# Kernel tuning notes

Hardware: AMD Instinct MI355X
Metric: run time of the kernel (lower is better)

Reference implementation:

```python
import jax, jax.numpy as jnp
import numpy as np

NQ = 4          # n_qubits
NL = 2          # ansatz layers in timestep circuit
T = 200         # n_timesteps
DEG = 3         # qsvt_degree
B = 2048        # batch
NROTS = 5 * NQ * NL     # 40
QFF_NROTS = 5 * NQ      # 20
DIM = 2 ** NQ

# --- batched 2x2 gate matrices (h = theta/2, shape (N,)) ---
def _rx(h):
    c = jnp.cos(h).astype(jnp.complex64)
    s = (-1j * jnp.sin(h)).astype(jnp.complex64)
    return jnp.stack([jnp.stack([c, s], -1), jnp.stack([s, c], -1)], -2)

def _ry(h):
    c, s = jnp.cos(h), jnp.sin(h)
    return jnp.stack([jnp.stack([c, -s], -1), jnp.stack([s, c], -1)], -2).astype(jnp.complex64)

def _rz(h):
    e = jnp.exp(-1j * h.astype(jnp.complex64))
    z = jnp.zeros_like(e)
    return jnp.stack([jnp.stack([e, z], -1), jnp.stack([z, jnp.conj(e)], -1)], -2)

# state layout: (N, 2, 2, ..., 2) with axis 1+w = qubit w (PennyLane wire ordering)
def _apply_1q(state, mat, w):
    st = jnp.moveaxis(state, 1 + w, -1)
    st = jnp.einsum('bij,b...j->b...i', mat, st)
    return jnp.moveaxis(st, -1, 1 + w)

def _apply_crx(state, h, cw, tw):
    m = _rx(h)
    st = jnp.moveaxis(state, (1 + cw, 1 + tw), (-2, -1))  # (..., control, target)
    s1 = jnp.einsum('bij,b...j->b...i', m, st[..., 1, :])  # RX on target iff control=1
    st = jnp.stack([st[..., 0, :], s1], axis=-2)
    return jnp.moveaxis(st, (-2, -1), (1 + cw, 1 + tw))

def _ansatz(state, params, layers):
    # params: (N, 5*NQ*layers) float
    half = params * 0.5
    idx = 0
    for _ in range(layers):
        for i in range(NQ):
            state = _apply_1q(state, _rx(half[:, idx]), i)
            state = _apply_1q(state, _ry(half[:, idx + 1]), i)
            state = _apply_1q(state, _rz(half[:, idx + 2]), i)
            idx += 3
        for i in range(NQ):
            state = _apply_crx(state, half[:, idx], i, (i + 1) % NQ)
            idx += 1
        for i in range(NQ - 1, -1, -1):
            state = _apply_crx(state, half[:, idx], i, (i - 1) % NQ)
            idx += 1
    return state

def _lcu(base, tparams, coeffs):
    # base: (B, DIM) complex; tparams: (B, T, NROTS); coeffs: (B, T) complex
    b, t, r = tparams.shape
    flat = tparams.reshape(b * t, r)
    st = jnp.repeat(base, t, axis=0).reshape((b * t,) + (2,) * NQ)
    st = _ansatz(st, flat, NL)
    ev = st.reshape(b, t, DIM)
    return jnp.einsum('bti,bt->bi', ev, coeffs)

def _expvals(state):
    # returns (B, 3*NQ): [<X_0..X_{n-1}>, <Y...>, <Z...>]
    outs_x, outs_y, outs_z = [], [], []
    red = tuple(range(1, NQ))  # reduce all non-batch, non-target axes after moveaxis
    for i in range(NQ):
        st = jnp.moveaxis(state, 1 + i, -1)
        s0, s1 = st[..., 0], st[..., 1]
        z = jnp.conj(s0) * s1
        outs_x.append(jnp.sum(2.0 * jnp.real(z), axis=red))
        outs_y.append(jnp.sum(2.0 * jnp.imag(z), axis=red))
        outs_z.append(jnp.sum(jnp.abs(s0) ** 2 - jnp.abs(s1) ** 2, axis=red))
    return jnp.stack(outs_x + outs_y + outs_z, axis=1).astype(jnp.float32)

def _forward(timestep_params, poly_coeffs, mix_re, mix_im, qff_params):
    b = timestep_params.shape[0]
    base = jnp.zeros((b, DIM), jnp.complex64).at[:, 0].set(1.0)
    coeffs = jnp.broadcast_to((mix_re + 1j * mix_im).astype(jnp.complex64), (b, T))
    # QSVT polynomial: acc = sum_k c_k (LCU)^k |0>
    acc = poly_coeffs[0] * base
    work = base
    for k in range(1, DEG + 1):
        work = _lcu(work, timestep_params, coeffs)
        acc = acc + poly_coeffs[k] * work
    acc = acc / jnp.sum(jnp.abs(poly_coeffs))  # L1 norm of poly coeffs
    norm = jnp.linalg.norm(acc, axis=1, keepdims=True)
    st = (acc / (norm + 1e-9)).reshape((b,) + (2,) * NQ)
    qp = jnp.broadcast_to(qff_params, (b, QFF_NROTS))
    st = _ansatz(st, qp, 1)
    return _expvals(st)

def setup_inputs() -> dict:
    key = jax.random.key(0)
    k1, k2, k3, k4, k5 = jax.random.split(key, 5)
    return {
        'timestep_params': jax.random.uniform(k1, (B, T, NROTS), jnp.float32),
        'poly_coeffs': jax.random.uniform(k2, (DEG + 1,), jnp.float32),
        'mix_re': jax.random.uniform(k3, (T,), jnp.float32),
        'mix_im': jax.random.uniform(k4, (T,), jnp.float32),
        'qff_params': jax.random.uniform(k5, (QFF_NROTS,), jnp.float32),
    }

def reference(timestep_params, poly_coeffs, mix_re, mix_im, qff_params):
    return _forward(timestep_params, poly_coeffs, mix_re, mix_im, qff_params)
```

## Files before the change

kernel.cpp:

```cpp
#include <hip/hip_runtime.h>
#include <math.h>

#define TSTEPS 200
#define NROTS  40
#define BLK    256
#define DEG    3

typedef float f2 __attribute__((ext_vector_type(2)));

__device__ __forceinline__ void fsc(float h, float& s, float& c) {
    s = __sinf(h); c = __cosf(h);
}

__device__ __forceinline__ f2 crot(f2 a) { return (f2){-a.y, a.x}; }

__device__ __forceinline__ void make_u(float h1, float h2, float h3, float* u) {
    float s1, c1, s2, c2, s3, c3;
    fsc(h1, s1, c1); fsc(h2, s2, c2); fsc(h3, s3, c3);
    float A = c1 * c2, Bv = s1 * s2, C = c1 * s2, D = s1 * c2;
    u[0] =  c3 * A + s3 * Bv;
    u[1] =  c3 * Bv - s3 * A;
    u[2] = -(c3 * C + s3 * D);
    u[3] =  s3 * C - c3 * D;
}

template<int BIT>
__device__ __forceinline__ void g_u2(f2* A, const float* u) {
    const float u00r = u[0], u00i = u[1], u01r = u[2], u01i = u[3];
    #pragma unroll
    for (int p = 0; p < 16; ++p) {
        if (p & BIT) continue;
        const int q = p | BIT;
        f2 a0 = A[p], a1 = A[q];
        f2 r0 = crot(a0), r1 = crot(a1);
        A[p] =  u00r * a0 + u00i * r0 + u01r * a1 + u01i * r1;
        A[q] =  u00r * a1 - u00i * r1 - u01r * a0 + u01i * r0;
    }
}

template<int CBIT, int TBIT>
__device__ __forceinline__ void g_crx_pre(f2* A, float s, float c) {
    #pragma unroll
    for (int p = 0; p < 16; ++p) {
        if (!(p & CBIT) || (p & TBIT)) continue;
        const int q = p | TBIT;
        f2 a0 = A[p], a1 = A[q];
        A[p] = c * a0 - s * crot(a1);
        A[q] = c * a1 - s * crot(a0);
    }
}

__device__ __forceinline__ void apply_layer_pre(f2* A, const float (&u)[4][4],
                                                const float (&cs)[8][2]) {
    g_u2<8>(A, u[0]); g_u2<4>(A, u[1]); g_u2<2>(A, u[2]); g_u2<1>(A, u[3]);
    g_crx_pre<8, 4>(A, cs[0][0], cs[0][1]);
    g_crx_pre<4, 2>(A, cs[1][0], cs[1][1]);
    g_crx_pre<2, 1>(A, cs[2][0], cs[2][1]);
    g_crx_pre<1, 8>(A, cs[3][0], cs[3][1]);
    g_crx_pre<1, 2>(A, cs[4][0], cs[4][1]);
    g_crx_pre<2, 4>(A, cs[5][0], cs[5][1]);
    g_crx_pre<4, 8>(A, cs[6][0], cs[6][1]);
    g_crx_pre<8, 1>(A, cs[7][0], cs[7][1]);
}

template<int S, int HALF>
__device__ __forceinline__ void rstep(f2* A, int lane) {
    const bool hi = (lane >> S) & 1;
    #pragma unroll
    for (int j = 0; j < HALF; ++j) {
        f2 send = hi ? A[j] : A[j + HALF];
        f2 keep = hi ? A[j + HALF] : A[j];
        f2 got;
        got.x = __shfl_xor(send.x, 1 << S, 64);
        got.y = __shfl_xor(send.y, 1 << S, 64);
        A[j] = keep + got;
    }
}

extern "C" __global__ void __launch_bounds__(BLK)
qac_kernel(const float* __restrict__ tp,
           const float* __restrict__ poly,
           const float* __restrict__ mixr,
           const float* __restrict__ mixi,
           const float* __restrict__ qff,
           float* __restrict__ out)
{
    __shared__ f2 s_red[4][16];
    __shared__ f2 s_w[16];
    __shared__ f2 s_acc[16];

    const int b    = blockIdx.x;
    const int tid  = threadIdx.x;
    const int lane = tid & 63;
    const int wv   = tid >> 6;

    if (tid < 16) {
        s_w[tid]   = (f2){tid == 0 ? 1.f : 0.f, 0.f};
        s_acc[tid] = (f2){tid == 0 ? poly[0] : 0.f, 0.f};
    }

    float cr_ = 0.f, ci_ = 0.f;
    if (tid < TSTEPS) { cr_ = mixr[tid]; ci_ = mixi[tid]; }
    const int mt = (tid < TSTEPS) ? tid : (TSTEPS - 1);
    const float4* p4 = (const float4*)(tp + (size_t)b * (TSTEPS * NROTS) + mt * NROTS);

    float tu[2][4][4];
    float tc[2][8][2];
    #pragma unroll
    for (int L = 0; L < 2; ++L) {
        float4 f0 = p4[5*L+0], f1 = p4[5*L+1], f2v = p4[5*L+2], f3 = p4[5*L+3], f4 = p4[5*L+4];
        make_u(0.5f*f0.x,  0.5f*f0.y,  0.5f*f0.z,  tu[L][0]);
        make_u(0.5f*f0.w,  0.5f*f1.x,  0.5f*f1.y,  tu[L][1]);
        make_u(0.5f*f1.z,  0.5f*f1.w,  0.5f*f2v.x, tu[L][2]);
        make_u(0.5f*f2v.y, 0.5f*f2v.z, 0.5f*f2v.w, tu[L][3]);
        fsc(0.5f*f3.x, tc[L][0][0], tc[L][0][1]);
        fsc(0.5f*f3.y, tc[L][1][0], tc[L][1][1]);
        fsc(0.5f*f3.z, tc[L][2][0], tc[L][2][1]);
        fsc(0.5f*f3.w, tc[L][3][0], tc[L][3][1]);
        fsc(0.5f*f4.x, tc[L][4][0], tc[L][4][1]);
        fsc(0.5f*f4.y, tc[L][5][0], tc[L][5][1]);
        fsc(0.5f*f4.z, tc[L][6][0], tc[L][6][1]);
        fsc(0.5f*f4.w, tc[L][7][0], tc[L][7][1]);
    }

    const int vidx = ((lane & 1) << 3) | ((lane & 2) << 1) | ((lane & 4) >> 1) | ((lane & 8) >> 3);

    __syncthreads();

    #pragma unroll 1
    for (int k = 1; k <= DEG; ++k) {
        f2 A[16];
        #pragma unroll
        for (int i = 0; i < 16; ++i) A[i] = s_w[i];

        apply_layer_pre(A, tu[0], tc[0]);
        apply_layer_pre(A, tu[1], tc[1]);

        #pragma unroll
        for (int i = 0; i < 16; ++i) A[i] = cr_ * A[i] + ci_ * crot(A[i]);

        rstep<0, 8>(A, lane);
        rstep<1, 4>(A, lane);
        rstep<2, 2>(A, lane);
        rstep<3, 1>(A, lane);
        f2 tot = A[0];
        tot.x += __shfl_xor(tot.x, 16, 64); tot.y += __shfl_xor(tot.y, 16, 64);
        tot.x += __shfl_xor(tot.x, 32, 64); tot.y += __shfl_xor(tot.y, 32, 64);
        if (lane < 16) s_red[wv][vidx] = tot;

        __syncthreads();
        if (tid < 16) {
            f2 r = s_red[0][tid] + s_red[1][tid] + s_red[2][tid] + s_red[3][tid];
            s_w[tid] = r;
            s_acc[tid] += poly[k] * r;
        }
        __syncthreads();
    }

    if (tid < 16) {
        const int l = tid;
        float l1 = fabsf(poly[0]) + fabsf(poly[1]) + fabsf(poly[2]) + fabsf(poly[3]);
        float inv = 1.f / l1;
        float ar = s_acc[l].x * inv, ai = s_acc[l].y * inv;
        float n2 = ar * ar + ai * ai;
        #pragma unroll
        for (int o = 1; o < 16; o <<= 1) n2 += __shfl_xor(n2, o, 64);
        float sc = 1.f / (sqrtf(n2) + 1e-9f);
        ar *= sc; ai *= sc;

        float s, c, pr, pi, se, ce, t0;
        #pragma unroll
        for (int w = 0; w < 4; ++w) {
            const int BIT = 8 >> w;
            fsc(0.5f * qff[3 * w + 0], s, c);
            pr = __shfl_xor(ar, BIT, 64); pi = __shfl_xor(ai, BIT, 64);
            t0 = c * ar + s * pi; ai = c * ai - s * pr; ar = t0;
            fsc(0.5f * qff[3 * w + 1], s, c);
            pr = __shfl_xor(ar, BIT, 64); pi = __shfl_xor(ai, BIT, 64);
            se = (l & BIT) ? s : -s;
            t0 = c * ar + se * pr; ai = c * ai + se * pi; ar = t0;
            fsc(0.5f * qff[3 * w + 2], s, c);
            se = (l & BIT) ? s : -s;
            t0 = c * ar - se * ai; ai = c * ai + se * ar; ar = t0;
        }
        #define CRXF(CB, TB, hp) { fsc(0.5f * (hp), s, c);                        \
            pr = __shfl_xor(ar, TB, 64); pi = __shfl_xor(ai, TB, 64);             \
            ce = (l & CB) ? c : 1.f; se = (l & CB) ? s : 0.f;                     \
            t0 = ce * ar + se * pi; ai = ce * ai - se * pr; ar = t0; }
        CRXF(8, 4, qff[12]) CRXF(4, 2, qff[13]) CRXF(2, 1, qff[14]) CRXF(1, 8, qff[15])
        CRXF(1, 2, qff[16]) CRXF(2, 4, qff[17]) CRXF(4, 8, qff[18]) CRXF(8, 1, qff[19])
        #undef CRXF

        float* o = out + (size_t)b * 12;
        #pragma unroll
        for (int w = 0; w < 4; ++w) {
            const int BIT = 8 >> w;
            pr = __shfl_xor(ar, BIT, 64); pi = __shfl_xor(ai, BIT, 64);
            float m = (l & BIT) ? 0.f : 1.f;
            float X = m * 2.f * (ar * pr + ai * pi);
            float Y = m * 2.f * (ar * pi - ai * pr);
            float Z = m * (ar * ar + ai * ai - pr * pr - pi * pi);
            #pragma unroll
            for (int of = 1; of < 16; of <<= 1) {
                X += __shfl_xor(X, of, 64);
                Y += __shfl_xor(Y, of, 64);
                Z += __shfl_xor(Z, of, 64);
            }
            if (l == 0) { o[w] = X; o[4 + w] = Y; o[8 + w] = Z; }
        }
    }
}

extern "C" void kernel_launch(void* const* d_in, const int* in_sizes, int n_in,
                              void* d_out, int out_size, void* d_ws, size_t ws_size,
                              hipStream_t stream) {
    const float* tp   = (const float*)d_in[0];
    const float* poly = (const float*)d_in[1];
    const float* mixr = (const float*)d_in[2];
    const float* mixi = (const float*)d_in[3];
    const float* qff  = (const float*)d_in[4];
    float* out = (float*)d_out;
    const int B = in_sizes[0] / (TSTEPS * NROTS);
    qac_kernel<<<dim3(B), dim3(BLK), 0, stream>>>(tp, poly, mixr, mixi, qff, out);
}
```

Baseline: 163.1 us.

## Switch state to split real/imag planes packed in pairs for packed FP32 math

Each thread's 16-amplitude state moves from interleaved complex values to separate real and imaginary planes. Each two-float vector now holds two neighbouring amplitudes, so gates on the upper three qubits can run as two-wide packed FP32 multiply-adds. Gates that act within a pair (qubit bit 1) get dedicated scalar routines, and the shared-memory accumulator is read back in planar order. The aim is to cut VALU instruction count in the gate-simulation loop, which dominates the kernel. The cost is more complex indexing and some extra lane extract/insert work for the intra-pair gates.

```diff
diff --git a/kernel.cpp b/kernel.cpp
--- a/kernel.cpp
+++ b/kernel.cpp
@@ -6,13 +6,13 @@
 #define BLK    256
 #define DEG    3
 
-typedef float f2 __attribute__((ext_vector_type(2)));
+typedef float f2v __attribute__((ext_vector_type(2)));
+
+__device__ __forceinline__ f2v vs(float x) { return (f2v){x, x}; }
 
 __device__ __forceinline__ void fsc(float h, float& s, float& c) {
     s = __sinf(h); c = __cosf(h);
 }
-
-__device__ __forceinline__ f2 crot(f2 a) { return (f2){-a.y, a.x}; }
 
 __device__ __forceinline__ void make_u(float h1, float h2, float h3, float* u) {
     float s1, c1, s2, c2, s3, c3;
@@ -24,56 +24,103 @@
     u[3] =  s3 * C - c3 * D;
 }
 
-template<int BIT>
-__device__ __forceinline__ void g_u2(f2* A, const float* u) {
+template<int PB>
+__device__ __forceinline__ void g_u2_pk(f2v* R, f2v* I, const float* u) {
+    const f2v u00r = vs(u[0]), u00i = vs(u[1]), u01r = vs(u[2]), u01i = vs(u[3]);
+    #pragma unroll
+    for (int pj = 0; pj < 8; ++pj) {
+        if (pj & PB) continue;
+        const int qj = pj | PB;
+        f2v a0r = R[pj], a0i = I[pj], a1r = R[qj], a1i = I[qj];
+        R[pj] =  u00r*a0r - u00i*a0i + u01r*a1r - u01i*a1i;
+        I[pj] =  u00r*a0i + u00i*a0r + u01r*a1i + u01i*a1r;
+        R[qj] = -(u01r*a0r) - u01i*a0i + u00r*a1r + u00i*a1i;
+        I[qj] = -(u01r*a0i) + u01i*a0r + u00r*a1i - u00i*a1r;
+    }
+}
+
+__device__ __forceinline__ void g_u2_b1(f2v* R, f2v* I, const float* u) {
     const float u00r = u[0], u00i = u[1], u01r = u[2], u01i = u[3];
     #pragma unroll
-    for (int p = 0; p < 16; ++p) {
-        if (p & BIT) continue;
-        const int q = p | BIT;
-        f2 a0 = A[p], a1 = A[q];
-        f2 r0 = crot(a0), r1 = crot(a1);
-        A[p] =  u00r * a0 + u00i * r0 + u01r * a1 + u01i * r1;
-        A[q] =  u00r * a1 - u00i * r1 - u01r * a0 + u01i * r0;
-    }
-}
-
-template<int CBIT, int TBIT>
-__device__ __forceinline__ void g_crx_pre(f2* A, float s, float c) {
-    #pragma unroll
-    for (int p = 0; p < 16; ++p) {
-        if (!(p & CBIT) || (p & TBIT)) continue;
-        const int q = p | TBIT;
-        f2 a0 = A[p], a1 = A[q];
-        A[p] = c * a0 - s * crot(a1);
-        A[q] = c * a1 - s * crot(a0);
-    }
-}
-
-__device__ __forceinline__ void apply_layer_pre(f2* A, const float (&u)[4][4],
-                                                const float (&cs)[8][2]) {
-    g_u2<8>(A, u[0]); g_u2<4>(A, u[1]); g_u2<2>(A, u[2]); g_u2<1>(A, u[3]);
-    g_crx_pre<8, 4>(A, cs[0][0], cs[0][1]);
-    g_crx_pre<4, 2>(A, cs[1][0], cs[1][1]);
-    g_crx_pre<2, 1>(A, cs[2][0], cs[2][1]);
-    g_crx_pre<1, 8>(A, cs[3][0], cs[3][1]);
-    g_crx_pre<1, 2>(A, cs[4][0], cs[4][1]);
-    g_crx_pre<2, 4>(A, cs[5][0], cs[5][1]);
-    g_crx_pre<4, 8>(A, cs[6][0], cs[6][1]);
-    g_crx_pre<8, 1>(A, cs[7][0], cs[7][1]);
+    for (int j = 0; j < 8; ++j) {
+        float a0r = R[j].x, a0i = I[j].x, a1r = R[j].y, a1i = I[j].y;
+        R[j].x =  u00r*a0r - u00i*a0i + u01r*a1r - u01i*a1i;
+        I[j].x =  u00r*a0i + u00i*a0r + u01r*a1i + u01i*a1r;
+        R[j].y = -u01r*a0r - u01i*a0i + u00r*a1r + u00i*a1i;
+        I[j].y = -u01r*a0i + u01i*a0r + u00r*a1i - u00i*a1r;
+    }
+}
+
+template<int PC, int PT>
+__device__ __forceinline__ void g_crx_pk(f2v* R, f2v* I, float s, float c) {
+    const f2v sv = vs(s), cv = vs(c);
+    #pragma unroll
+    for (int pj = 0; pj < 8; ++pj) {
+        if (!(pj & PC) || (pj & PT)) continue;
+        const int qj = pj | PT;
+        f2v a0r = R[pj], a0i = I[pj], a1r = R[qj], a1i = I[qj];
+        R[pj] = cv*a0r + sv*a1i;
+        I[pj] = cv*a0i - sv*a1r;
+        R[qj] = cv*a1r + sv*a0i;
+        I[qj] = cv*a1i - sv*a0r;
+    }
+}
+
+template<int JC>
+__device__ __forceinline__ void g_crx_t1(f2v* R, f2v* I, float s, float c) {
+    #pragma unroll
+    for (int j = 0; j < 8; ++j) {
+        if (!(j & JC)) continue;
+        float a0r = R[j].x, a0i = I[j].x, a1r = R[j].y, a1i = I[j].y;
+        R[j].x = c*a0r + s*a1i;
+        I[j].x = c*a0i - s*a1r;
+        R[j].y = c*a1r + s*a0i;
+        I[j].y = c*a1i - s*a0r;
+    }
+}
+
+template<int PT>
+__device__ __forceinline__ void g_crx_c1(f2v* R, f2v* I, float s, float c) {
+    #pragma unroll
+    for (int j = 0; j < 8; ++j) {
+        if (j & PT) continue;
+        const int qj = j | PT;
+        float a0r = R[j].y, a0i = I[j].y, a1r = R[qj].y, a1i = I[qj].y;
+        R[j].y  = c*a0r + s*a1i;
+        I[j].y  = c*a0i - s*a1r;
+        R[qj].y = c*a1r + s*a0i;
+        I[qj].y = c*a1i - s*a0r;
+    }
+}
+
+__device__ __forceinline__ void apply_layer_pk(f2v* R, f2v* I,
+                                               const float (&u)[4][4],
+                                               const float (&cs)[8][2]) {
+    g_u2_pk<4>(R, I, u[0]);
+    g_u2_pk<2>(R, I, u[1]);
+    g_u2_pk<1>(R, I, u[2]);
+    g_u2_b1  (R, I, u[3]);
+    g_crx_pk<4, 2>(R, I, cs[0][0], cs[0][1]);
+    g_crx_pk<2, 1>(R, I, cs[1][0], cs[1][1]);
+    g_crx_t1<1>   (R, I, cs[2][0], cs[2][1]);
+    g_crx_c1<4>   (R, I, cs[3][0], cs[3][1]);
+    g_crx_c1<1>   (R, I, cs[4][0], cs[4][1]);
+    g_crx_pk<1, 2>(R, I, cs[5][0], cs[5][1]);
+    g_crx_pk<2, 4>(R, I, cs[6][0], cs[6][1]);
+    g_crx_t1<4>   (R, I, cs[7][0], cs[7][1]);
 }
 
 template<int S, int HALF>
-__device__ __forceinline__ void rstep(f2* A, int lane) {
+__device__ __forceinline__ void rstep_pk(f2v* W, int lane) {
     const bool hi = (lane >> S) & 1;
     #pragma unroll
     for (int j = 0; j < HALF; ++j) {
-        f2 send = hi ? A[j] : A[j + HALF];
-        f2 keep = hi ? A[j + HALF] : A[j];
-        f2 got;
+        f2v send = hi ? W[j] : W[j + HALF];
+        f2v keep = hi ? W[j + HALF] : W[j];
+        f2v got;
         got.x = __shfl_xor(send.x, 1 << S, 64);
         got.y = __shfl_xor(send.y, 1 << S, 64);
-        A[j] = keep + got;
+        W[j] = keep + got;
     }
 }
 
@@ -85,9 +132,9 @@
            const float* __restrict__ qff,
            float* __restrict__ out)
 {
-    __shared__ f2 s_red[4][16];
-    __shared__ f2 s_w[16];
-    __shared__ f2 s_acc[16];
+    __shared__ f2v s_redP[4][16];
+    __shared__ f2v s_wP[16];
+    __shared__ f2v s_accP[16];
 
     const int b    = blockIdx.x;
     const int tid  = threadIdx.x;
@@ -95,8 +142,8 @@
     const int wv   = tid >> 6;
 
     if (tid < 16) {
-        s_w[tid]   = (f2){tid == 0 ? 1.f : 0.f, 0.f};
-        s_acc[tid] = (f2){tid == 0 ? poly[0] : 0.f, 0.f};
+        s_wP[tid]   = (f2v){tid == 0 ? 1.f : 0.f, 0.f};
+        s_accP[tid] = (f2v){tid == 0 ? poly[0] : 0.f, 0.f};
     }
 
     float cr_ = 0.f, ci_ = 0.f;
@@ -108,11 +155,11 @@
     float tc[2][8][2];
     #pragma unroll
     for (int L = 0; L < 2; ++L) {
-        float4 f0 = p4[5*L+0], f1 = p4[5*L+1], f2v = p4[5*L+2], f3 = p4[5*L+3], f4 = p4[5*L+4];
+        float4 f0 = p4[5*L+0], f1 = p4[5*L+1], f2q = p4[5*L+2], f3 = p4[5*L+3], f4 = p4[5*L+4];
         make_u(0.5f*f0.x,  0.5f*f0.y,  0.5f*f0.z,  tu[L][0]);
         make_u(0.5f*f0.w,  0.5f*f1.x,  0.5f*f1.y,  tu[L][1]);
-        make_u(0.5f*f1.z,  0.5f*f1.w,  0.5f*f2v.x, tu[L][2]);
-        make_u(0.5f*f2v.y, 0.5f*f2v.z, 0.5f*f2v.w, tu[L][3]);
+        make_u(0.5f*f1.z,  0.5f*f1.w,  0.5f*f2q.x, tu[L][2]);
+        make_u(0.5f*f2q.y, 0.5f*f2q.z, 0.5f*f2q.w, tu[L][3]);
         fsc(0.5f*f3.x, tc[L][0][0], tc[L][0][1]);
         fsc(0.5f*f3.y, tc[L][1][0], tc[L][1][1]);
         fsc(0.5f*f3.z, tc[L][2][0], tc[L][2][1]);
@@ -129,39 +176,44 @@
 
     #pragma unroll 1
     for (int k = 1; k <= DEG; ++k) {
-        f2 A[16];
-        #pragma unroll
-        for (int i = 0; i < 16; ++i) A[i] = s_w[i];
-
-        apply_layer_pre(A, tu[0], tc[0]);
-        apply_layer_pre(A, tu[1], tc[1]);
-
-        #pragma unroll
-        for (int i = 0; i < 16; ++i) A[i] = cr_ * A[i] + ci_ * crot(A[i]);
-
-        rstep<0, 8>(A, lane);
-        rstep<1, 4>(A, lane);
-        rstep<2, 2>(A, lane);
-        rstep<3, 1>(A, lane);
-        f2 tot = A[0];
+        f2v W[16];
+        #pragma unroll
+        for (int j = 0; j < 16; ++j) W[j] = s_wP[j];
+
+        apply_layer_pk(W, W + 8, tu[0], tc[0]);
+        apply_layer_pk(W, W + 8, tu[1], tc[1]);
+
+        #pragma unroll
+        for (int j = 0; j < 8; ++j) {
+            f2v r = W[j], im = W[8 + j];
+            W[j]     = vs(cr_)*r - vs(ci_)*im;
+            W[8 + j] = vs(ci_)*r + vs(cr_)*im;
+        }
+
+        rstep_pk<0, 8>(W, lane);
+        rstep_pk<1, 4>(W, lane);
+        rstep_pk<2, 2>(W, lane);
+        rstep_pk<3, 1>(W, lane);
+        f2v tot = W[0];
         tot.x += __shfl_xor(tot.x, 16, 64); tot.y += __shfl_xor(tot.y, 16, 64);
         tot.x += __shfl_xor(tot.x, 32, 64); tot.y += __shfl_xor(tot.y, 32, 64);
-        if (lane < 16) s_red[wv][vidx] = tot;
+        if (lane < 16) s_redP[wv][vidx] = tot;
 
         __syncthreads();
         if (tid < 16) {
-            f2 r = s_red[0][tid] + s_red[1][tid] + s_red[2][tid] + s_red[3][tid];
-            s_w[tid] = r;
-            s_acc[tid] += poly[k] * r;
+            f2v r = s_redP[0][tid] + s_redP[1][tid] + s_redP[2][tid] + s_redP[3][tid];
+            s_wP[tid] = r;
+            s_accP[tid] += vs(poly[k]) * r;
         }
         __syncthreads();
     }
 
     if (tid < 16) {
         const int l = tid;
+        const float* accf = (const float*)s_accP;
         float l1 = fabsf(poly[0]) + fabsf(poly[1]) + fabsf(poly[2]) + fabsf(poly[3]);
         float inv = 1.f / l1;
-        float ar = s_acc[l].x * inv, ai = s_acc[l].y * inv;
+        float ar = accf[l] * inv, ai = accf[16 + l] * inv;
         float n2 = ar * ar + ai * ai;
         #pragma unroll
         for (int o = 1; o < 16; o <<= 1) n2 += __shfl_xor(n2, o, 64);
```

New measurement: 184.1 us. 12.8% more time.
